# Kernel tuning notes

Hardware: AMD Instinct MI355X
Metric: run time of the kernel (lower is better)

Reference implementation:

```python
import jax, jax.numpy as jnp
import numpy as np

BS, N, NP, K = 2, 4096, 1024, 8   # batch, fine pts, coarse pts, in-degree per fine node
CI, CO, MID = 32, 16, 32          # in channels (16 skip + 16 interpolated), out channels, radial MLP width
E = BS * N * K


def setup_inputs() -> dict:
    key = jax.random.key(0)
    ks = iter(jax.random.split(key, 64))
    nrm = lambda s, sc=1.0: jax.random.normal(next(ks), s, jnp.float32) * sc
    inp = {}
    inp['h0'] = nrm((BS * N, 16, 1))
    inp['h1'] = nrm((BS * N, 16, 3))
    inp['uph0'] = nrm((BS * NP, 16, 1))
    inp['uph1'] = nrm((BS * NP, 16, 3))
    inp['xyz'] = jax.random.uniform(next(ks), (BS, N, 3), jnp.float32)
    inp['xyz_prev'] = jax.random.uniform(next(ks), (BS, NP, 3), jnp.float32)
    dst = jnp.repeat(jnp.arange(BS * N, dtype=jnp.int32), K)
    src = (dst // N) * N + jax.random.randint(next(ks), (E,), 0, N, jnp.int32)
    inp['edge_src'], inp['edge_dst'] = src, dst
    xf = inp['xyz'].reshape(BS * N, 3)
    inp['r'] = jnp.linalg.norm(xf[src] - xf[dst], axis=-1, keepdims=True)
    # CG basis tensors basis[din,dout]: [E, 2*dout+1, 2*din+1, 2*min(din,dout)+1]
    inp['basis00'] = nrm((E, 1, 1, 1))
    inp['basis01'] = nrm((E, 3, 1, 1))
    inp['basis10'] = nrm((E, 1, 3, 1))
    inp['basis11'] = nrm((E, 3, 3, 3))
    for p, f in (('00', 1), ('01', 1), ('10', 1), ('11', 3)):
        inp['rw1_' + p] = nrm((1, MID), 0.5)
        inp['rb1_' + p] = jnp.zeros((MID,), jnp.float32)
        inp['rw2_' + p] = nrm((MID, MID), 0.2)
        inp['rb2_' + p] = jnp.zeros((MID,), jnp.float32)
        inp['rw3_' + p] = nrm((MID, CO * CI * f), 0.1)
    inp['wself0'] = nrm((CO, CI), 0.1)
    inp['wself1'] = nrm((CO, CI), 0.1)
    inp['gamma0'] = jnp.ones((CO,), jnp.float32)
    inp['beta0'] = jnp.zeros((CO,), jnp.float32)
    inp['gamma1'] = jnp.ones((CO,), jnp.float32)
    inp['beta1'] = jnp.zeros((CO,), jnp.float32)
    return inp


def _radial(r, w1, b1, w2, b2, w3, f):
    x = jax.nn.relu(r @ w1 + b1)
    x = jax.nn.relu(x @ w2 + b2)
    return (x @ w3).reshape(E, CO, CI, f)


def _pair_msg(basis, hsrc, R):
    # basis [E,mo,mi,f], hsrc [E,ci,mi], R [E,co,ci,f] -> msg [E,co,mo]
    # (fused form of per-edge kernel = sum_f R*basis followed by kernel @ src)
    tmp = jnp.einsum('emnf,ein->eimf', basis, hsrc)
    return jnp.einsum('eoif,eimf->eom', R, tmp)


def _gnorm(h, gamma, beta):
    # GNormSE3: norm over m-dim, LayerNorm+ReLU on norms, rescale phase
    n = jnp.sqrt(jnp.sum(h * h, -1) + 1e-12)           # [Nn,co]
    phase = h / n[..., None]
    mu = jnp.mean(n, -1, keepdims=True)
    var = jnp.var(n, -1, keepdims=True)
    t = jax.nn.relu((n - mu) / jnp.sqrt(var + 1e-5) * gamma + beta)
    return t[..., None] * phase


def _fwd(h0, h1, uph0, uph1, xyz, xyz_prev, r, basis00, basis01, basis10, basis11,
         rw1_00, rb1_00, rw2_00, rb2_00, rw3_00,
         rw1_01, rb1_01, rw2_01, rb2_01, rw3_01,
         rw1_10, rb1_10, rw2_10, rb2_10, rw3_10,
         rw1_11, rb1_11, rw2_11, rb2_11, rw3_11,
         wself0, wself1, gamma0, beta0, gamma1, beta1, edge_src, edge_dst):
    # --- three_nn + inverse-squared-distance interpolation of coarse features ---
    d2 = jnp.sum((xyz[:, :, None, :] - xyz_prev[:, None, :, :]) ** 2, -1)  # [B,N,NP]
    negd, idx = jax.lax.top_k(-d2, 3)
    dist = jnp.sqrt(jnp.maximum(-negd, 0.0))
    d2c = jnp.maximum(dist * dist, 1e-10)
    inv = 1.0 / (d2c + 1e-8)
    w = inv / jnp.sum(inv, -1, keepdims=True)          # [B,N,3]

    def interp(uph):
        C, F = uph.shape[1], uph.shape[2]
        fp = uph.reshape(BS, NP, C * F)
        g = jax.vmap(lambda f_, i_: f_[i_])(fp, idx)   # [B,N,3,C*F]
        return jnp.sum(g * w[..., None], 2).reshape(BS * N, C, F)

    h0c = jnp.concatenate([interp(uph0), h0], 1)       # [BN,CI,1]
    h1c = jnp.concatenate([interp(uph1), h1], 1)       # [BN,CI,3]

    # --- GConvSE3: per-edge CG-basis kernels, mean aggregation, self-interaction ---
    hs0, hs1 = h0c[edge_src], h1c[edge_src]
    R00 = _radial(r, rw1_00, rb1_00, rw2_00, rb2_00, rw3_00, 1)
    R01 = _radial(r, rw1_01, rb1_01, rw2_01, rb2_01, rw3_01, 1)
    R10 = _radial(r, rw1_10, rb1_10, rw2_10, rb2_10, rw3_10, 1)
    R11 = _radial(r, rw1_11, rb1_11, rw2_11, rb2_11, rw3_11, 3)
    msg0 = _pair_msg(basis00, hs0, R00) + _pair_msg(basis10, hs1, R10)  # [E,CO,1]
    msg1 = _pair_msg(basis01, hs0, R01) + _pair_msg(basis11, hs1, R11)  # [E,CO,3]
    agg0 = jax.ops.segment_sum(msg0, edge_dst, num_segments=BS * N) / K  # mean (in-degree K)
    agg1 = jax.ops.segment_sum(msg1, edge_dst, num_segments=BS * N) / K
    out0 = agg0 + jnp.einsum('oi,nim->nom', wself0, h0c)
    out1 = agg1 + jnp.einsum('oi,nim->nom', wself1, h1c)

    return _gnorm(out0, gamma0, beta0), _gnorm(out1, gamma1, beta1)


def reference(h0, h1, uph0, uph1, xyz, xyz_prev, r, basis00, basis01, basis10, basis11,
              rw1_00, rb1_00, rw2_00, rb2_00, rw3_00,
              rw1_01, rb1_01, rw2_01, rb2_01, rw3_01,
              rw1_10, rb1_10, rw2_10, rb2_10, rw3_10,
              rw1_11, rb1_11, rw2_11, rb2_11, rw3_11,
              wself0, wself1, gamma0, beta0, gamma1, beta1, edge_src, edge_dst):
    return _fwd(h0, h1, uph0, uph1, xyz, xyz_prev, r, basis00, basis01, basis10, basis11,
                rw1_00, rb1_00, rw2_00, rb2_00, rw3_00,
                rw1_01, rb1_01, rw2_01, rb2_01, rw3_01,
                rw1_10, rb1_10, rw2_10, rb2_10, rw3_10,
                rw1_11, rb1_11, rw2_11, rb2_11, rw3_11,
                wself0, wself1, gamma0, beta0, gamma1, beta1, edge_src, edge_dst)
```

## Files before the change

### kernel.cpp

```cpp
#include <hip/hip_runtime.h>
#include <hip/hip_bf16.h>
#include <hip/hip_fp16.h>
#include <math.h>

#define NPP   1024
#define BN    8192
#define NE    65536

typedef __attribute__((ext_vector_type(8))) short bf16x8;
typedef __attribute__((ext_vector_type(4))) float f32x4;

__device__ __forceinline__ short f2bf(float f) {
  __hip_bfloat16 h = __float2bfloat16(f);
  return *reinterpret_cast<short*>(&h);
}
__device__ __forceinline__ float b2f(short h) {
  unsigned u = ((unsigned)(unsigned short)h) << 16;
  return __uint_as_float(u);
}
__device__ __forceinline__ unsigned short f2h(float f) {
  __half h = __float2half(f);
  return *reinterpret_cast<unsigned short*>(&h);
}
__device__ __forceinline__ float h2f(unsigned short u) {
  __half h = *reinterpret_cast<__half*>(&u);
  return __half2float(h);
}

__device__ __forceinline__ unsigned long long pkkey(float d, int j) {
  return ((unsigned long long)__float_as_uint(d) << 32) | (unsigned int)j;
}

__global__ __launch_bounds__(256) void prolog_kernel(
    const float* __restrict__ h0, const float* __restrict__ h1,
    const float* __restrict__ uph0, const float* __restrict__ uph1,
    const float* __restrict__ xyz, const float* __restrict__ xyzp,
    float* __restrict__ h0c, float* __restrict__ h1c,
    const float* __restrict__ w00, const float* __restrict__ w01,
    const float* __restrict__ w10, const float* __restrict__ w11,
    const float* __restrict__ w2_00, const float* __restrict__ w2_01,
    const float* __restrict__ w2_10, const float* __restrict__ w2_11,
    unsigned short* __restrict__ B00, unsigned short* __restrict__ B01,
    unsigned short* __restrict__ B10, unsigned short* __restrict__ B11,
    unsigned short* __restrict__ W2H, unsigned short* __restrict__ W2L)
{
  const int tid = threadIdx.x;
  if (blockIdx.x >= BN/4) {
    int idx = (blockIdx.x - BN/4) * 256 + tid;
    if (idx < 49152) {
      int a = idx & 16383;
      int i = a & 31, o = (a >> 5) & 15, k = a >> 9;
      int src = k*512 + o*32 + i;
      if (idx < 16384)      B00[a] = (unsigned short)f2bf(w00[src]);
      else if (idx < 32768) B01[a] = (unsigned short)f2bf(w01[src]);
      else                  B10[a] = (unsigned short)f2bf(w10[src]);
    } else if (idx < 98304) {
      int a = idx - 49152;
      int i = a & 31, o = (a >> 5) & 15, s = a >> 9;
      int f = s >> 5, k = s & 31;
      B11[a] = (unsigned short)f2bf(w11[k*1536 + (o*32+i)*3 + f]);
    } else if (idx < 102400) {
      int a = idx - 98304;
      int p = a >> 10, rem = a & 1023;
      int b = rem >> 5, aa = rem & 31;
      const float* w2p = p==0?w2_00 : p==1?w2_01 : p==2?w2_10 : w2_11;
      W2H[a] = (unsigned short)f2bf(w2p[aa*32 + b]);
    } else if (idx < 106496) {
      int a = idx - 102400;
      int p = a >> 10, rem = a & 1023;
      int b = rem >> 5, aa = rem & 31;
      const float* w2p = p==0?w2_00 : p==1?w2_01 : p==2?w2_10 : w2_11;
      float v = w2p[aa*32 + b];
      short h = f2bf(v);
      W2L[a] = (unsigned short)f2bf(v - b2f(h));
    }
    return;
  }

  const int lane = tid & 63;
  const int wid  = tid >> 6;
  const int fi   = blockIdx.x * 4 + wid;
  const int b    = fi >> 12;

  const float px = xyz[fi*3+0], py = xyz[fi*3+1], pz = xyz[fi*3+2];

  unsigned long long k0 = ~0ull, k1 = ~0ull, k2 = ~0ull;
  const float* cbase = xyzp + (size_t)b*NPP*3;
  #pragma unroll 4
  for (int j = lane; j < NPP; j += 64) {
    const float* cp = cbase + j*3;
    float ax = px - cp[0], ay = py - cp[1], az = pz - cp[2];
    float dd = fmaf(az, az, fmaf(ay, ay, ax*ax));
    unsigned long long kk = pkkey(dd, j);
    if (kk < k0)      { k2 = k1; k1 = k0; k0 = kk; }
    else if (kk < k1) { k2 = k1; k1 = kk; }
    else if (kk < k2) { k2 = kk; }
  }
  #pragma unroll
  for (int off = 1; off < 64; off <<= 1) {
    unsigned long long b0 = __shfl_xor(k0, off);
    unsigned long long b1 = __shfl_xor(k1, off);
    unsigned long long b2 = __shfl_xor(k2, off);
    unsigned long long c0, c1, c2;
    if (k0 <= b0) {
      c0 = k0;
      if (k1 <= b0) { c1 = k1; c2 = (k2 <= b0) ? k2 : b0; }
      else          { c1 = b0; c2 = (k1 <= b1) ? k1 : b1; }
    } else {
      c0 = b0;
      if (b1 <= k0) { c1 = b1; c2 = (b2 <= k0) ? b2 : k0; }
      else          { c1 = k0; c2 = (b1 <= k1) ? b1 : k1; }
    }
    k0 = c0; k1 = c1; k2 = c2;
  }
  const int i0 = (int)(k0 & 0xffffffffu);
  const int i1 = (int)(k1 & 0xffffffffu);
  const int i2 = (int)(k2 & 0xffffffffu);
  const float dd0 = __uint_as_float((unsigned)(k0 >> 32));
  const float dd1 = __uint_as_float((unsigned)(k1 >> 32));
  const float dd2 = __uint_as_float((unsigned)(k2 >> 32));

  float w0, w1v, w2v;
  {
    float s0 = sqrtf(fmaxf(dd0, 0.f));
    float s1 = sqrtf(fmaxf(dd1, 0.f));
    float s2 = sqrtf(fmaxf(dd2, 0.f));
    w0  = 1.f / (fmaxf(s0*s0, 1e-10f) + 1e-8f);
    w1v = 1.f / (fmaxf(s1*s1, 1e-10f) + 1e-8f);
    w2v = 1.f / (fmaxf(s2*s2, 1e-10f) + 1e-8f);
    float wsum = w0 + w1v + w2v;
    w0 /= wsum; w1v /= wsum; w2v /= wsum;
  }

  const float* u0 = uph0 + (size_t)b*NPP*16;
  const float* u1 = uph1 + (size_t)b*NPP*48;
  if (lane < 16) {
    int c = lane;
    h0c[(size_t)fi*32 + c] = w0*u0[i0*16+c] + w1v*u0[i1*16+c] + w2v*u0[i2*16+c];
    h0c[(size_t)fi*32 + 16 + c] = h0[(size_t)fi*16 + c];
  } else {
    int q = lane - 16;
    h1c[(size_t)fi*96 + q] = w0*u1[i0*48+q] + w1v*u1[i1*48+q] + w2v*u1[i2*48+q];
    h1c[(size_t)fi*96 + 48 + q] = h1[(size_t)fi*48 + q];
  }
}

struct EP {
  const float *r; const int *esrc;
  const float *b00, *b01, *b10, *b11;
  const float *w1_00, *b1_00, *b2_00;
  const float *w1_01, *b1_01, *b2_01;
  const float *w1_10, *b1_10, *b2_10;
  const float *w1_11, *b1_11, *b2_11;
  const unsigned short *B00, *B01, *B10, *B11, *W2H, *W2L;
  const float *h0c, *h1c;
  float *agg0, *agg1;
};

#define CVT4(PTR) ({ ushort4 u_ = *(const ushort4*)(PTR); \
    f32x4 r_; r_[0]=h2f(u_.x); r_[1]=h2f(u_.y); r_[2]=h2f(u_.z); r_[3]=h2f(u_.w); r_; })

__global__ __launch_bounds__(256) void edge_mfma(EP P)
{
  __shared__ __align__(16) unsigned short x2Lh[32*264];

  const int tid  = threadIdx.x;
  const int wid  = tid >> 6;
  const int lane = tid & 63;
  const int el   = lane & 15;
  const int kg   = lane >> 4;
  const int kg4  = kg << 2;
  const int eb   = blockIdx.x * 64 + wid * 16;
  const int e    = eb + el;
  const int isl  = kg * 8;

  const int   sidx = P.esrc[e];
  const float rv   = P.r[e];

  const f32x4 zero4 = {0.f, 0.f, 0.f, 0.f};

  #pragma unroll
  for (int p = 0; p < 4; ++p) {
    const float* w1p = p==0?P.w1_00 : p==1?P.w1_01 : p==2?P.w1_10 : P.w1_11;
    const float* b1p = p==0?P.b1_00 : p==1?P.b1_01 : p==2?P.b1_10 : P.b1_11;
    const float* b2p = p==0?P.b2_00 : p==1?P.b2_01 : p==2?P.b2_10 : P.b2_11;
    const unsigned short* w2hp = P.W2H + p*1024;
    const unsigned short* w2lp = P.W2L + p*1024;
    f32x4 wa  = *(const f32x4*)(w1p + isl);
    f32x4 wb  = *(const f32x4*)(w1p + isl + 4);
    f32x4 ba  = *(const f32x4*)(b1p + isl);
    f32x4 bbv = *(const f32x4*)(b1p + isl + 4);
    bf16x8 bh0 = *(const bf16x8*)(w2hp + el*32 + isl);
    bf16x8 bh1 = *(const bf16x8*)(w2hp + (16+el)*32 + isl);
    bf16x8 bl0 = *(const bf16x8*)(w2lp + el*32 + isl);
    bf16x8 bl1 = *(const bf16x8*)(w2lp + (16+el)*32 + isl);
    float b2v0 = b2p[el];
    float b2v1 = b2p[16 + el];
    bf16x8 axh, axl;
    #pragma unroll
    for (int j = 0; j < 4; ++j) {
      float v0 = fmaxf(fmaf(rv, wa[j], ba[j]),  0.f);
      float v1 = fmaxf(fmaf(rv, wb[j], bbv[j]), 0.f);
      short h0s = f2bf(v0), h1s_ = f2bf(v1);
      axh[j]   = h0s;  axl[j]   = f2bf(v0 - b2f(h0s));
      axh[j+4] = h1s_; axl[j+4] = f2bf(v1 - b2f(h1s_));
    }
    f32x4 z0 = __builtin_amdgcn_mfma_f32_16x16x32_bf16(axl, bh0, zero4, 0,0,0);
    z0 = __builtin_amdgcn_mfma_f32_16x16x32_bf16(axh, bl0, z0, 0,0,0);
    z0 = __builtin_amdgcn_mfma_f32_16x16x32_bf16(axh, bh0, z0, 0,0,0);
    f32x4 z1 = __builtin_amdgcn_mfma_f32_16x16x32_bf16(axl, bh1, zero4, 0,0,0);
    z1 = __builtin_amdgcn_mfma_f32_16x16x32_bf16(axh, bl1, z1, 0,0,0);
    z1 = __builtin_amdgcn_mfma_f32_16x16x32_bf16(axh, bh1, z1, 0,0,0);
    ushort4 o0, o1v;
    o0.x  = f2h(fmaxf(z0[0] + b2v0, 0.f));
    o0.y  = f2h(fmaxf(z0[1] + b2v0, 0.f));
    o0.z  = f2h(fmaxf(z0[2] + b2v0, 0.f));
    o0.w  = f2h(fmaxf(z0[3] + b2v0, 0.f));
    o1v.x = f2h(fmaxf(z1[0] + b2v1, 0.f));
    o1v.y = f2h(fmaxf(z1[1] + b2v1, 0.f));
    o1v.z = f2h(fmaxf(z1[2] + b2v1, 0.f));
    o1v.w = f2h(fmaxf(z1[3] + b2v1, 0.f));
    *(ushort4*)&x2Lh[el*264      + wid*64 + p*16 + kg4] = o0;
    *(ushort4*)&x2Lh[(16+el)*264 + wid*64 + p*16 + kg4] = o1v;
  }

  f32x4 h0a = *(const f32x4*)(P.h0c + (size_t)sidx*32 + isl);
  f32x4 h0b = *(const f32x4*)(P.h0c + (size_t)sidx*32 + isl + 4);
  float h1sl[24];
  {
    const float* hp = P.h1c + (size_t)sidx*96 + isl*3;
    #pragma unroll
    for (int q = 0; q < 6; ++q) {
      f32x4 v = *(const f32x4*)(hp + q*4);
      h1sl[q*4+0]=v[0]; h1sl[q*4+1]=v[1]; h1sl[q*4+2]=v[2]; h1sl[q*4+3]=v[3];
    }
  }

  bf16x8 a_h0;
  #pragma unroll
  for (int j = 0; j < 4; ++j) { a_h0[j] = f2bf(h0a[j]); a_h0[j+4] = f2bf(h0b[j]); }

  bf16x8 a_t;
  {
    const float* bp = P.b10 + (size_t)e*3;
    float c0 = bp[0], c1 = bp[1], c2 = bp[2];
    #pragma unroll
    for (int j = 0; j < 8; ++j)
      a_t[j] = f2bf(c0*h1sl[j*3+0] + c1*h1sl[j*3+1] + c2*h1sl[j*3+2]);
  }

  const int xrow = wid*64 + kg4;

  f32x4 macc00 = zero4, c01 = zero4, macc10 = zero4;
  {
    const unsigned short* bb00 = P.B00 + el*32 + isl;
    const unsigned short* bb01 = P.B01 + el*32 + isl;
    const unsigned short* bb10 = P.B10 + el*32 + isl;
    #pragma unroll 2
    for (int t = 0; t < 32; ++t) {
      bf16x8 bv00 = *(const bf16x8*)(bb00 + t*512);
      bf16x8 bv01 = *(const bf16x8*)(bb01 + t*512);
      bf16x8 bv10 = *(const bf16x8*)(bb10 + t*512);
      f32x4 xs0 = CVT4(&x2Lh[t*264 + xrow + 0]);
      f32x4 xs1 = CVT4(&x2Lh[t*264 + xrow + 16]);
      f32x4 xs2 = CVT4(&x2Lh[t*264 + xrow + 32]);
      f32x4 z00 = __builtin_amdgcn_mfma_f32_16x16x32_bf16(a_h0, bv00, zero4, 0, 0, 0);
      f32x4 z01 = __builtin_amdgcn_mfma_f32_16x16x32_bf16(a_h0, bv01, zero4, 0, 0, 0);
      f32x4 z10 = __builtin_amdgcn_mfma_f32_16x16x32_bf16(a_t,  bv10, zero4, 0, 0, 0);
      macc00[0] = fmaf(xs0[0], z00[0], macc00[0]);
      macc00[1] = fmaf(xs0[1], z00[1], macc00[1]);
      macc00[2] = fmaf(xs0[2], z00[2], macc00[2]);
      macc00[3] = fmaf(xs0[3], z00[3], macc00[3]);
      c01[0] = fmaf(xs1[0], z01[0], c01[0]);
      c01[1] = fmaf(xs1[1], z01[1], c01[1]);
      c01[2] = fmaf(xs1[2], z01[2], c01[2]);
      c01[3] = fmaf(xs1[3], z01[3], c01[3]);
      macc10[0] = fmaf(xs2[0], z10[0], macc10[0]);
      macc10[1] = fmaf(xs2[1], z10[1], macc10[1]);
      macc10[2] = fmaf(xs2[2], z10[2], macc10[2]);
      macc10[3] = fmaf(xs2[3], z10[3], macc10[3]);
    }
  }
  {
    f32x4 bv = *(const f32x4*)(P.b00 + eb + kg4);
    float s = fmaf(bv[0], macc00[0], macc10[0])
            + fmaf(bv[1], macc00[1], macc10[1])
            + fmaf(bv[2], macc00[2], macc10[2])
            + fmaf(bv[3], macc00[3], macc10[3]);
    s += __shfl_xor(s, 16);
    if ((kg & 1) == 0)
      P.agg0[(size_t)((eb >> 3) + (kg >> 1))*16 + el] = s * 0.125f;
  }

  f32x4 m1a, m1b, m1c;
  {
    const float* bp = P.b01 + (size_t)(eb + kg4)*3;
    f32x4 q0 = *(const f32x4*)(bp);
    f32x4 q1 = *(const f32x4*)(bp + 4);
    f32x4 q2 = *(const f32x4*)(bp + 8);
    m1a[0]=c01[0]*q0[0]; m1a[1]=c01[1]*q0[3]; m1a[2]=c01[2]*q1[2]; m1a[3]=c01[3]*q2[1];
    m1b[0]=c01[0]*q0[1]; m1b[1]=c01[1]*q1[0]; m1b[2]=c01[2]*q1[3]; m1b[3]=c01[3]*q2[2];
    m1c[0]=c01[0]*q0[2]; m1c[1]=c01[1]*q1[1]; m1c[2]=c01[2]*q2[0]; m1c[3]=c01[3]*q2[3];
  }

  {
    bf16x8 am[3][3];
    const float* b11e = P.b11 + (size_t)e*27;
    #pragma unroll
    for (int f = 0; f < 3; ++f) {
      float bm[9];
      #pragma unroll
      for (int mn = 0; mn < 9; ++mn) bm[mn] = b11e[mn*3 + f];
      #pragma unroll
      for (int j = 0; j < 8; ++j) {
        float hn0 = h1sl[j*3+0], hn1 = h1sl[j*3+1], hn2 = h1sl[j*3+2];
        am[f][0][j] = f2bf(bm[0]*hn0 + bm[1]*hn1 + bm[2]*hn2);
        am[f][1][j] = f2bf(bm[3]*hn0 + bm[4]*hn1 + bm[5]*hn2);
        am[f][2][j] = f2bf(bm[6]*hn0 + bm[7]*hn1 + bm[8]*hn2);
      }
    }
    const unsigned short* bb = P.B11 + el*32 + isl;
    #pragma unroll 4
    for (int t = 0; t < 32; ++t) {
      bf16x8 bv0 = *(const bf16x8*)(bb + t*512);
      bf16x8 bv1 = *(const bf16x8*)(bb + 16384 + t*512);
      bf16x8 bv2 = *(const bf16x8*)(bb + 32768 + t*512);
      f32x4 xs = CVT4(&x2Lh[t*264 + xrow + 48]);
      #pragma unroll
      for (int f = 0; f < 3; ++f) {
        bf16x8 bv = f==0 ? bv0 : (f==1 ? bv1 : bv2);
        f32x4 z0 = __builtin_amdgcn_mfma_f32_16x16x32_bf16(am[f][0], bv, zero4, 0, 0, 0);
        f32x4 z1 = __builtin_amdgcn_mfma_f32_16x16x32_bf16(am[f][1], bv, zero4, 0, 0, 0);
        f32x4 z2 = __builtin_amdgcn_mfma_f32_16x16x32_bf16(am[f][2], bv, zero4, 0, 0, 0);
        m1a[0] = fmaf(xs[0], z0[0], m1a[0]);
        m1a[1] = fmaf(xs[1], z0[1], m1a[1]);
        m1a[2] = fmaf(xs[2], z0[2], m1a[2]);
        m1a[3] = fmaf(xs[3], z0[3], m1a[3]);
        m1b[0] = fmaf(xs[0], z1[0], m1b[0]);
        m1b[1] = fmaf(xs[1], z1[1], m1b[1]);
        m1b[2] = fmaf(xs[2], z1[2], m1b[2]);
        m1b[3] = fmaf(xs[3], z1[3], m1b[3]);
        m1c[0] = fmaf(xs[0], z2[0], m1c[0]);
        m1c[1] = fmaf(xs[1], z2[1], m1c[1]);
        m1c[2] = fmaf(xs[2], z2[2], m1c[2]);
        m1c[3] = fmaf(xs[3], z2[3], m1c[3]);
      }
    }
  }

  {
    float sa = m1a[0]+m1a[1]+m1a[2]+m1a[3]; sa += __shfl_xor(sa, 16);
    float sb = m1b[0]+m1b[1]+m1b[2]+m1b[3]; sb += __shfl_xor(sb, 16);
    float sc = m1c[0]+m1c[1]+m1c[2]+m1c[3]; sc += __shfl_xor(sc, 16);
    if ((kg & 1) == 0) {
      float* p = P.agg1 + (size_t)((eb >> 3) + (kg >> 1))*48 + el*3;
      p[0] = sa * 0.125f; p[1] = sb * 0.125f; p[2] = sc * 0.125f;
    }
  }
}

__global__ __launch_bounds__(256) void gnorm_kernel(
    const float* __restrict__ agg0, const float* __restrict__ agg1,
    const float* __restrict__ h0c, const float* __restrict__ h1c,
    const float* __restrict__ ws0, const float* __restrict__ ws1,
    const float* __restrict__ g0, const float* __restrict__ be0,
    const float* __restrict__ g1, const float* __restrict__ be1,
    float* __restrict__ out)
{
  const int gt  = blockIdx.x * 256 + threadIdx.x;
  const int fi  = gt >> 2;
  const int t4  = gt & 3;
  const int ob  = t4 * 4;

  const float* h0p = h0c + (size_t)fi*32;
  const float* h1p = h1c + (size_t)fi*96;

  float o0[4];
  #pragma unroll
  for (int oo = 0; oo < 4; ++oo) {
    int o = ob + oo;
    float a = agg0[(size_t)fi*16 + o];
    #pragma unroll
    for (int i = 0; i < 32; ++i)
      a = fmaf(ws0[o*32+i], h0p[i], a);
    o0[oo] = a;
  }
  {
    float n0[4], lmu = 0.f;
    #pragma unroll
    for (int oo = 0; oo < 4; ++oo) { n0[oo] = sqrtf(fmaf(o0[oo], o0[oo], 1e-12f)); lmu += n0[oo]; }
    lmu += __shfl_xor(lmu, 1); lmu += __shfl_xor(lmu, 2);
    float mu = lmu * 0.0625f;
    float lv = 0.f;
    #pragma unroll
    for (int oo = 0; oo < 4; ++oo) { float d = n0[oo]-mu; lv = fmaf(d, d, lv); }
    lv += __shfl_xor(lv, 1); lv += __shfl_xor(lv, 2);
    float inv = 1.f / sqrtf(lv * 0.0625f + 1e-5f);
    #pragma unroll
    for (int oo = 0; oo < 4; ++oo) {
      int o = ob + oo;
      float t = fmaxf(fmaf((n0[oo]-mu)*inv, g0[o], be0[o]), 0.f);
      out[(size_t)fi*16 + o] = t * (o0[oo] / n0[oo]);
    }
  }

  float o1[12];
  #pragma unroll
  for (int oo = 0; oo < 4; ++oo) {
    int o = ob + oo;
    float a0 = agg1[(size_t)fi*48 + o*3+0];
    float a1 = agg1[(size_t)fi*48 + o*3+1];
    float a2 = agg1[(size_t)fi*48 + o*3+2];
    #pragma unroll
    for (int i = 0; i < 32; ++i) {
      float wv = ws1[o*32+i];
      a0 = fmaf(wv, h1p[i*3+0], a0);
      a1 = fmaf(wv, h1p[i*3+1], a1);
      a2 = fmaf(wv, h1p[i*3+2], a2);
    }
    o1[oo*3+0] = a0; o1[oo*3+1] = a1; o1[oo*3+2] = a2;
  }
  {
    float n1[4], lmu = 0.f;
    #pragma unroll
    for (int oo = 0; oo < 4; ++oo) {
      float s = fmaf(o1[oo*3+0], o1[oo*3+0], 1e-12f);
      s = fmaf(o1[oo*3+1], o1[oo*3+1], s);
      s = fmaf(o1[oo*3+2], o1[oo*3+2], s);
      n1[oo] = sqrtf(s); lmu += n1[oo];
    }
    lmu += __shfl_xor(lmu, 1); lmu += __shfl_xor(lmu, 2);
    float mu = lmu * 0.0625f;
    float lv = 0.f;
    #pragma unroll
    for (int oo = 0; oo < 4; ++oo) { float d = n1[oo]-mu; lv = fmaf(d, d, lv); }
    lv += __shfl_xor(lv, 1); lv += __shfl_xor(lv, 2);
    float inv = 1.f / sqrtf(lv * 0.0625f + 1e-5f);
    float* out1 = out + (size_t)BN*16;
    #pragma unroll
    for (int oo = 0; oo < 4; ++oo) {
      int o = ob + oo;
      float t = fmaxf(fmaf((n1[oo]-mu)*inv, g1[o], be1[o]), 0.f);
      #pragma unroll
      for (int m = 0; m < 3; ++m)
        out1[(size_t)fi*48 + o*3+m] = t * (o1[oo*3+m] / n1[oo]);
    }
  }
}

extern "C" void kernel_launch(void* const* d_in, const int* in_sizes, int n_in,
                              void* d_out, int out_size, void* d_ws, size_t ws_size,
                              hipStream_t stream)
{
  (void)in_sizes; (void)n_in; (void)out_size; (void)ws_size;
  const float* h0   = (const float*)d_in[0];
  const float* h1   = (const float*)d_in[1];
  const float* uph0 = (const float*)d_in[2];
  const float* uph1 = (const float*)d_in[3];
  const float* xyz  = (const float*)d_in[4];
  const float* xyzp = (const float*)d_in[5];
  const int*   esrc = (const int*)d_in[6];
  const float* rr   = (const float*)d_in[8];

  float* wsp  = (float*)d_ws;
  float* h0c  = wsp;
  float* h1c  = h0c + (size_t)BN*32;
  float* agg0 = h1c + (size_t)BN*96;
  float* agg1 = agg0 + (size_t)BN*16;
  unsigned short* B00 = (unsigned short*)(agg1 + (size_t)BN*48);
  unsigned short* B01 = B00 + 16384;
  unsigned short* B10 = B01 + 16384;
  unsigned short* B11 = B10 + 16384;
  unsigned short* W2H = B11 + 49152;
  unsigned short* W2L = W2H + 4096;

  prolog_kernel<<<BN/4 + 416, 256, 0, stream>>>(
      h0, h1, uph0, uph1, xyz, xyzp, h0c, h1c,
      (const float*)d_in[17], (const float*)d_in[22],
      (const float*)d_in[27], (const float*)d_in[32],
      (const float*)d_in[15], (const float*)d_in[20],
      (const float*)d_in[25], (const float*)d_in[30],
      B00, B01, B10, B11, W2H, W2L);

  EP P;
  P.r = rr; P.esrc = esrc;
  P.b00 = (const float*)d_in[9];  P.b01 = (const float*)d_in[10];
  P.b10 = (const float*)d_in[11]; P.b11 = (const float*)d_in[12];
  P.w1_00 = (const float*)d_in[13]; P.b1_00 = (const float*)d_in[14]; P.b2_00 = (const float*)d_in[16];
  P.w1_01 = (const float*)d_in[18]; P.b1_01 = (const float*)d_in[19]; P.b2_01 = (const float*)d_in[21];
  P.w1_10 = (const float*)d_in[23]; P.b1_10 = (const float*)d_in[24]; P.b2_10 = (const float*)d_in[26];
  P.w1_11 = (const float*)d_in[28]; P.b1_11 = (const float*)d_in[29]; P.b2_11 = (const float*)d_in[31];
  P.B00 = B00; P.B01 = B01; P.B10 = B10; P.B11 = B11; P.W2H = W2H; P.W2L = W2L;
  P.h0c = h0c; P.h1c = h1c; P.agg0 = agg0; P.agg1 = agg1;

  edge_mfma<<<NE/64, 256, 0, stream>>>(P);

  gnorm_kernel<<<BN*4/256, 256, 0, stream>>>(agg0, agg1, h0c, h1c,
      (const float*)d_in[33], (const float*)d_in[34],
      (const float*)d_in[35], (const float*)d_in[36],
      (const float*)d_in[37], (const float*)d_in[38],
      (float*)d_out);
}
```

Baseline: 101.5 us.

## Stage radial weight tiles into LDS with double-buffered direct global-to-LDS loads

The weight matrices B00/B01/B10/B11 were previously read by every wave straight from global memory inside the t-loops. Now the block cooperatively stages 4-step chunks into a double-buffered LDS array using global_load_lds, prefetching the next chunk while computing on the current one, with a barrier per chunk. The x2Lh row stride also changes from 264 to 260. This cuts redundant per-wave global and L2 traffic but adds barriers and about 24KB of LDS, which may lower occupancy.

```diff
diff --git a/kernel.cpp b/kernel.cpp
--- a/kernel.cpp
+++ b/kernel.cpp
@@ -162,7 +162,8 @@
 
 __global__ __launch_bounds__(256) void edge_mfma(EP P)
 {
-  __shared__ __align__(16) unsigned short x2Lh[32*264];
+  __shared__ __align__(16) unsigned short x2Lh[32*260];
+  __shared__ __align__(16) unsigned short Bst[2][12*512];
 
   const int tid  = threadIdx.x;
   const int wid  = tid >> 6;
@@ -178,6 +179,27 @@
   const float rv   = P.r[e];
 
   const f32x4 zero4 = {0.f, 0.f, 0.f, 0.f};
+
+  auto stage_chunk = [&](int c, int bufi) {
+    #pragma unroll
+    for (int i = 0; i < 3; ++i) {
+      const int j = wid*3 + i;
+      const int sub = j >> 2, tloc = j & 3;
+      const unsigned short* src;
+      if (c < 8) {
+        const unsigned short* Bp = (sub == 0) ? P.B00 : ((sub == 1) ? P.B01 : P.B10);
+        src = Bp + (size_t)(c*4 + tloc)*512 + el*32 + isl;
+      } else {
+        src = P.B11 + (size_t)sub*16384 + (size_t)((c-8)*4 + tloc)*512 + el*32 + isl;
+      }
+      __builtin_amdgcn_global_load_lds(
+          (const __attribute__((address_space(1))) unsigned int*)src,
+          (__attribute__((address_space(3))) unsigned int*)&Bst[bufi][j*512],
+          16, 0, 0);
+    }
+  };
+
+  stage_chunk(0, 0);
 
   #pragma unroll
   for (int p = 0; p < 4; ++p) {
@@ -220,8 +242,8 @@
     o1v.y = f2h(fmaxf(z1[1] + b2v1, 0.f));
     o1v.z = f2h(fmaxf(z1[2] + b2v1, 0.f));
     o1v.w = f2h(fmaxf(z1[3] + b2v1, 0.f));
-    *(ushort4*)&x2Lh[el*264      + wid*64 + p*16 + kg4] = o0;
-    *(ushort4*)&x2Lh[(16+el)*264 + wid*64 + p*16 + kg4] = o1v;
+    *(ushort4*)&x2Lh[el*260      + wid*64 + p*16 + kg4] = o0;
+    *(ushort4*)&x2Lh[(16+el)*260 + wid*64 + p*16 + kg4] = o1v;
   }
 
   f32x4 h0a = *(const f32x4*)(P.h0c + (size_t)sidx*32 + isl);
@@ -251,19 +273,23 @@
 
   const int xrow = wid*64 + kg4;
 
+  __syncthreads();
+  int buf = 0;
+
   f32x4 macc00 = zero4, c01 = zero4, macc10 = zero4;
-  {
-    const unsigned short* bb00 = P.B00 + el*32 + isl;
-    const unsigned short* bb01 = P.B01 + el*32 + isl;
-    const unsigned short* bb10 = P.B10 + el*32 + isl;
-    #pragma unroll 2
-    for (int t = 0; t < 32; ++t) {
-      bf16x8 bv00 = *(const bf16x8*)(bb00 + t*512);
-      bf16x8 bv01 = *(const bf16x8*)(bb01 + t*512);
-      bf16x8 bv10 = *(const bf16x8*)(bb10 + t*512);
-      f32x4 xs0 = CVT4(&x2Lh[t*264 + xrow + 0]);
-      f32x4 xs1 = CVT4(&x2Lh[t*264 + xrow + 16]);
-      f32x4 xs2 = CVT4(&x2Lh[t*264 + xrow + 32]);
+  #pragma unroll 1
+  for (int c = 0; c < 8; ++c) {
+    stage_chunk(c + 1, buf ^ 1);
+    const unsigned short* Bb = &Bst[buf][0];
+    #pragma unroll
+    for (int tl = 0; tl < 4; ++tl) {
+      const int t = c*4 + tl;
+      bf16x8 bv00 = *(const bf16x8*)&Bb[(0*4 + tl)*512 + lane*8];
+      bf16x8 bv01 = *(const bf16x8*)&Bb[(1*4 + tl)*512 + lane*8];
+      bf16x8 bv10 = *(const bf16x8*)&Bb[(2*4 + tl)*512 + lane*8];
+      f32x4 xs0 = CVT4(&x2Lh[t*260 + xrow + 0]);
+      f32x4 xs1 = CVT4(&x2Lh[t*260 + xrow + 16]);
+      f32x4 xs2 = CVT4(&x2Lh[t*260 + xrow + 32]);
       f32x4 z00 = __builtin_amdgcn_mfma_f32_16x16x32_bf16(a_h0, bv00, zero4, 0, 0, 0);
       f32x4 z01 = __builtin_amdgcn_mfma_f32_16x16x32_bf16(a_h0, bv01, zero4, 0, 0, 0);
       f32x4 z10 = __builtin_amdgcn_mfma_f32_16x16x32_bf16(a_t,  bv10, zero4, 0, 0, 0);
@@ -280,7 +306,10 @@
       macc10[2] = fmaf(xs2[2], z10[2], macc10[2]);
       macc10[3] = fmaf(xs2[3], z10[3], macc10[3]);
     }
-  }
+    __syncthreads();
+    buf ^= 1;
+  }
+
   {
     f32x4 bv = *(const f32x4*)(P.b00 + eb + kg4);
     float s = fmaf(bv[0], macc00[0], macc10[0])
@@ -319,32 +348,38 @@
         am[f][2][j] = f2bf(bm[6]*hn0 + bm[7]*hn1 + bm[8]*hn2);
       }
     }
-    const unsigned short* bb = P.B11 + el*32 + isl;
-    #pragma unroll 4
-    for (int t = 0; t < 32; ++t) {
-      bf16x8 bv0 = *(const bf16x8*)(bb + t*512);
-      bf16x8 bv1 = *(const bf16x8*)(bb + 16384 + t*512);
-      bf16x8 bv2 = *(const bf16x8*)(bb + 32768 + t*512);
-      f32x4 xs = CVT4(&x2Lh[t*264 + xrow + 48]);
+    #pragma unroll 1
+    for (int cc = 0; cc < 8; ++cc) {
+      if (cc < 7) stage_chunk(9 + cc, buf ^ 1);
+      const unsigned short* Bb = &Bst[buf][0];
       #pragma unroll
-      for (int f = 0; f < 3; ++f) {
-        bf16x8 bv = f==0 ? bv0 : (f==1 ? bv1 : bv2);
-        f32x4 z0 = __builtin_amdgcn_mfma_f32_16x16x32_bf16(am[f][0], bv, zero4, 0, 0, 0);
-        f32x4 z1 = __builtin_amdgcn_mfma_f32_16x16x32_bf16(am[f][1], bv, zero4, 0, 0, 0);
-        f32x4 z2 = __builtin_amdgcn_mfma_f32_16x16x32_bf16(am[f][2], bv, zero4, 0, 0, 0);
-        m1a[0] = fmaf(xs[0], z0[0], m1a[0]);
-        m1a[1] = fmaf(xs[1], z0[1], m1a[1]);
-        m1a[2] = fmaf(xs[2], z0[2], m1a[2]);
-        m1a[3] = fmaf(xs[3], z0[3], m1a[3]);
-        m1b[0] = fmaf(xs[0], z1[0], m1b[0]);
-        m1b[1] = fmaf(xs[1], z1[1], m1b[1]);
-        m1b[2] = fmaf(xs[2], z1[2], m1b[2]);
-        m1b[3] = fmaf(xs[3], z1[3], m1b[3]);
-        m1c[0] = fmaf(xs[0], z2[0], m1c[0]);
-        m1c[1] = fmaf(xs[1], z2[1], m1c[1]);
-        m1c[2] = fmaf(xs[2], z2[2], m1c[2]);
-        m1c[3] = fmaf(xs[3], z2[3], m1c[3]);
+      for (int tl = 0; tl < 4; ++tl) {
+        const int t = cc*4 + tl;
+        bf16x8 bv0 = *(const bf16x8*)&Bb[(0*4 + tl)*512 + lane*8];
+        bf16x8 bv1 = *(const bf16x8*)&Bb[(1*4 + tl)*512 + lane*8];
+        bf16x8 bv2 = *(const bf16x8*)&Bb[(2*4 + tl)*512 + lane*8];
+        f32x4 xs = CVT4(&x2Lh[t*260 + xrow + 48]);
+        #pragma unroll
+        for (int f = 0; f < 3; ++f) {
+          bf16x8 bv = f==0 ? bv0 : (f==1 ? bv1 : bv2);
+          f32x4 z0 = __builtin_amdgcn_mfma_f32_16x16x32_bf16(am[f][0], bv, zero4, 0, 0, 0);
+          f32x4 z1 = __builtin_amdgcn_mfma_f32_16x16x32_bf16(am[f][1], bv, zero4, 0, 0, 0);
+          f32x4 z2 = __builtin_amdgcn_mfma_f32_16x16x32_bf16(am[f][2], bv, zero4, 0, 0, 0);
+          m1a[0] = fmaf(xs[0], z0[0], m1a[0]);
+          m1a[1] = fmaf(xs[1], z0[1], m1a[1]);
+          m1a[2] = fmaf(xs[2], z0[2], m1a[2]);
+          m1a[3] = fmaf(xs[3], z0[3], m1a[3]);
+          m1b[0] = fmaf(xs[0], z1[0], m1b[0]);
+          m1b[1] = fmaf(xs[1], z1[1], m1b[1]);
+          m1b[2] = fmaf(xs[2], z1[2], m1b[2]);
+          m1b[3] = fmaf(xs[3], z1[3], m1b[3]);
+          m1c[0] = fmaf(xs[0], z2[0], m1c[0]);
+          m1c[1] = fmaf(xs[1], z2[1], m1c[1]);
+          m1c[2] = fmaf(xs[2], z2[2], m1c[2]);
+          m1c[3] = fmaf(xs[3], z2[3], m1c[3]);
+        }
       }
+      if (cc < 7) { __syncthreads(); buf ^= 1; }
     }
   }
 
```

Result: slower. 124.5 us (+22.7%).
